# Kernel optimization log

Measured on AMD Instinct MI355X. Metric: run time of the kernel, lower is better.

## Reference

```python
import jax, jax.numpy as jnp
import numpy as np

INV_SCALE = 1.0 / (0.5 * 9)  # module's inv_scale_factor; qk is DIVIDED by this (i.e. * 4.5)


def setup_inputs() -> dict:
    key0 = jax.random.key(0)
    ks = jax.random.split(key0, 8)
    B, Sq, Sk, D, Dv = 8, 2048, 2048, 128, 256
    return {
        "query": jax.random.normal(ks[0], (B, Sq, D), dtype=jnp.float32),
        "key": jax.random.normal(ks[1], (B, Sk, D), dtype=jnp.float32),
        "value": jax.random.normal(ks[2], (B, Sk, Dv), dtype=jnp.float32),
        "mask": jax.random.normal(ks[3], (B, Sq, Sk), dtype=jnp.float32),
        # Linear weights stored torch-style as [out_features, in_features]
        "W0": jax.random.normal(ks[4], (D, D), dtype=jnp.float32) * (1.0 / np.sqrt(D)),
        "W1": jax.random.normal(ks[5], (D, D), dtype=jnp.float32) * (1.0 / np.sqrt(D)),
        "W2": jax.random.normal(ks[6], (D, Dv), dtype=jnp.float32) * (1.0 / np.sqrt(Dv)),
        "Wout": jax.random.normal(ks[7], (Dv, D), dtype=jnp.float32) * (1.0 / np.sqrt(D)),
    }


def reference(query, key, value, mask, W0, W1, W2, Wout):
    r1 = jnp.einsum("bqd,od->bqo", query, W0)          # [B,Sq,128]
    r2 = jnp.einsum("bkd,od->bko", key, W1)            # [B,Sk,128]
    r3 = jnp.einsum("bkv,ov->bko", value, W2)          # [B,Sk,128]
    qk = jnp.einsum("bqd,bkd->bqk", r1, r2)            # [B,Sq,Sk]
    scaled_qk = qk / INV_SCALE
    softmax_qk = jax.nn.softmax(scaled_qk, axis=-1)
    # dropout is identity in eval mode (deterministic reference)
    v1 = jnp.einsum("bqk,bko->bqo", softmax_qk, r3)    # [B,Sq,128]
    v2 = jnp.einsum("bqo,vo->bqv", v1, Wout)           # [B,Sq,256]
    output = v2 + jnp.einsum("bqk,bkv->bqv", mask, value)
    return output
```

## Files before the change

kernel.cpp:

```cpp
#include <hip/hip_runtime.h>
#include <cstdint>

typedef __attribute__((ext_vector_type(8))) __bf16 bf16x8;
typedef __attribute__((ext_vector_type(4))) __bf16 bf16x4;
typedef __attribute__((ext_vector_type(4))) float f32x4;

#define MFMA16(a, b, c) __builtin_amdgcn_mfma_f32_16x16x32_bf16((a), (b), (c), 0, 0, 0)
#define WAITV(N) asm volatile("s_waitcnt vmcnt(" #N ")" ::: "memory")

static constexpr int SEQ = 2048;
static constexpr int DV = 256;
static constexpr float QK_SCALE = 4.5f;

__device__ __forceinline__ bf16x4 cvt4(float4 v) {
    bf16x4 y;
    y[0] = (__bf16)v.x; y[1] = (__bf16)v.y; y[2] = (__bf16)v.z; y[3] = (__bf16)v.w;
    return y;
}

__device__ __forceinline__ void gl_lds16(const void* g, void* l) {
    __builtin_amdgcn_global_load_lds((const __attribute__((address_space(1))) uint32_t*)g,
                                     (__attribute__((address_space(3))) uint32_t*)l, 16, 0, 0);
}

template <int K, int TRANS>
__global__ __launch_bounds__(256) void k_proj(const float* __restrict__ X,
                                              const float* __restrict__ W,
                                              __bf16* __restrict__ out,
                                              float outScale) {
    __shared__ __bf16 ldsX[64][136];
    __shared__ __bf16 ldsW[128][136];

    const int t = threadIdx.x;
    const int m0 = blockIdx.x * 64;
    const int w = t >> 6, l = t & 63, lrow = l & 15, lq = l >> 4;

    f32x4 acc[8];
#pragma unroll
    for (int i = 0; i < 8; ++i) acc[i] = f32x4{0.f, 0.f, 0.f, 0.f};

#pragma unroll
    for (int kh = 0; kh < K / 128; ++kh) {
        if (kh) __syncthreads();
#pragma unroll
        for (int i = 0; i < 8; ++i) {
            int idx = t + i * 256;
            int r = idx >> 5, c4 = idx & 31;
            float4 v = *(const float4*)(X + (size_t)(m0 + r) * K + kh * 128 + c4 * 4);
            *(bf16x4*)&ldsX[r][c4 * 4] = cvt4(v);
        }
#pragma unroll
        for (int i = 0; i < 16; ++i) {
            int idx = t + i * 256;
            int r = idx >> 5, c4 = idx & 31;
            float4 v = *(const float4*)(W + (size_t)r * K + kh * 128 + c4 * 4);
            *(bf16x4*)&ldsW[r][c4 * 4] = cvt4(v);
        }
        __syncthreads();

        bf16x8 aA[4];
#pragma unroll
        for (int kc = 0; kc < 4; ++kc)
            aA[kc] = *(const bf16x8*)((const char*)&ldsX[w * 16 + lrow][0] + kc * 64 + lq * 16);
#pragma unroll
        for (int nt = 0; nt < 8; ++nt) {
#pragma unroll
            for (int kc = 0; kc < 4; ++kc) {
                bf16x8 bB = *(const bf16x8*)((const char*)&ldsW[nt * 16 + lrow][0] + kc * 64 + lq * 16);
                acc[nt] = MFMA16(aA[kc], bB, acc[nt]);
            }
        }
    }

#pragma unroll
    for (int nt = 0; nt < 8; ++nt) {
        if (TRANS) {
            int gm = m0 + w * 16 + lq * 4;
            int b = gm >> 11, s = gm & 2047;
            int col = nt * 16 + lrow;
            int kt = s >> 5, s32 = s & 31;
            int slot = (s32 >> 3) ^ ((col >> 1) & 3);
            bf16x4 y;
#pragma unroll
            for (int j = 0; j < 4; ++j) y[j] = (__bf16)(acc[nt][j] * outScale);
            *(bf16x4*)(out + (((size_t)b * 64 + kt) * 128 + col) * 32 + slot * 8 + (s32 & 7)) = y;
        } else {
#pragma unroll
            for (int j = 0; j < 4; ++j) {
                int gm = m0 + w * 16 + lq * 4 + j;
                int col = nt * 16 + lrow;
                out[(size_t)gm * 128 + col] = (__bf16)(acc[nt][j] * outScale);
            }
        }
    }
}

__global__ __launch_bounds__(256) void k_vt(const float* __restrict__ V, __bf16* __restrict__ vt) {
    __shared__ __bf16 tile[64][72];
    const int t = threadIdx.x;
    const int b = blockIdx.z, s0 = blockIdx.x * 64, v0 = blockIdx.y * 64;
#pragma unroll
    for (int i = 0; i < 4; ++i) {
        int idx = t + i * 256;
        int r = idx >> 4, c4 = idx & 15;
        float4 x = *(const float4*)(V + ((size_t)b * SEQ + s0 + r) * DV + v0 + c4 * 4);
        *(bf16x4*)&tile[r][c4 * 4] = cvt4(x);
    }
    __syncthreads();
#pragma unroll
    for (int i = 0; i < 4; ++i) {
        int idx = t + i * 256;
        int vv = idx >> 4, c4 = idx & 15;
        bf16x4 y;
        y[0] = tile[c4 * 4 + 0][vv]; y[1] = tile[c4 * 4 + 1][vv];
        y[2] = tile[c4 * 4 + 2][vv]; y[3] = tile[c4 * 4 + 3][vv];
        int v = v0 + vv;
        int kt = (s0 >> 5) + (c4 >> 3);
        int slot = ((c4 >> 1) & 3) ^ ((v >> 1) & 3);
        *(bf16x4*)(vt + (((size_t)b * 64 + kt) * 256 + v) * 32 + slot * 8 + (c4 & 1) * 4) = y;
    }
}

__global__ __launch_bounds__(256) void k_cvt_bf16(const float* __restrict__ src,
                                                  __bf16* __restrict__ dst, int n4) {
    int i = blockIdx.x * 256 + threadIdx.x;
    if (i < n4) {
        float4 v = *(const float4*)(src + (size_t)i * 4);
        *(bf16x4*)(dst + (size_t)i * 4) = cvt4(v);
    }
}

__global__ __launch_bounds__(256) void k_flash(const __bf16* __restrict__ r1s,
                                               const __bf16* __restrict__ r2,
                                               const __bf16* __restrict__ r3p,
                                               __bf16* __restrict__ v1) {
    __shared__ __align__(16) __bf16 r2s[4][32 * 128];
    __shared__ __align__(16) __bf16 r3s[4][128 * 32];
    __shared__ __bf16 plds[4][16][48];

    const int t = threadIdx.x;
    const int bx = (int)((blockIdx.x & 7) * 32 + (blockIdx.x >> 3));
    const int b = bx >> 5, q0 = (bx & 31) * 64;
    const int w = t >> 6, l = t & 63, lrow = l & 15, lq = l >> 4;

    const __bf16* r1b = r1s + (size_t)b * SEQ * 128;
    const __bf16* r2b = r2 + (size_t)b * SEQ * 128;
    const __bf16* r3b = r3p + (size_t)b * 64 * 128 * 32;

    bf16x8 aQ[4];
    {
        const __bf16* p = r1b + (size_t)(q0 + w * 16 + lrow) * 128 + lq * 8;
#pragma unroll
        for (int kc = 0; kc < 4; ++kc) aQ[kc] = *(const bf16x8*)(p + kc * 32);
    }

    const __bf16* p_r2[2];
    const __bf16* p_r3[2];
#pragma unroll
    for (int q1 = 0; q1 < 2; ++q1) {
        int r = 8 * w + 4 * q1 + (l >> 4);
        int c = (l & 15) ^ (r & 15);
        p_r2[q1] = r2b + (size_t)r * 128 + c * 8;
        p_r3[q1] = r3b + (size_t)(2 * w + q1) * 512 + l * 8;
    }

    auto stage = [&](int bi) {
#pragma unroll
        for (int q1 = 0; q1 < 2; ++q1) {
            gl_lds16(p_r2[q1], &r2s[bi][(2 * w + q1) * 512]);
            gl_lds16(p_r3[q1], &r3s[bi][(2 * w + q1) * 512]);
            p_r2[q1] += 32 * 128;
            p_r3[q1] += 128 * 32;
        }
    };

    f32x4 acc[8];
#pragma unroll
    for (int i = 0; i < 8; ++i) acc[i] = f32x4{0.f, 0.f, 0.f, 0.f};
    float mrow[4] = {-INFINITY, -INFINITY, -INFINITY, -INFINITY};
    float lsum[4] = {0.f, 0.f, 0.f, 0.f};

    stage(0); stage(1); stage(2);
    for (int it = 0; it < 64; ++it) {
        if (it < 62) { WAITV(8); } else if (it == 62) { WAITV(4); } else { WAITV(0); }
        __builtin_amdgcn_s_barrier();
        __builtin_amdgcn_sched_barrier(0);
        if (it + 3 < 64) stage((it + 3) & 3);
        __builtin_amdgcn_sched_barrier(0);
        const __bf16* R2 = &r2s[it & 3][0];
        const __bf16* R3 = &r3s[it & 3][0];

        f32x4 sc[2];
#pragma unroll
        for (int ct = 0; ct < 2; ++ct) {
            f32x4 s = f32x4{0.f, 0.f, 0.f, 0.f};
#pragma unroll
            for (int kc = 0; kc < 4; ++kc) {
                int p = (kc * 4 + lq) ^ lrow;
                bf16x8 bb = *(const bf16x8*)&R2[(ct * 16 + lrow) * 128 + p * 8];
                s = MFMA16(aQ[kc], bb, s);
            }
            sc[ct] = s;
        }

        float pm[4], ps[4], al[4];
#pragma unroll
        for (int j = 0; j < 4; ++j) pm[j] = fmaxf(sc[0][j], sc[1][j]);
#pragma unroll
        for (int off = 1; off <= 8; off <<= 1)
#pragma unroll
            for (int j = 0; j < 4; ++j) pm[j] = fmaxf(pm[j], __shfl_xor(pm[j], off, 64));
#pragma unroll
        for (int j = 0; j < 4; ++j) {
            float mn = fmaxf(mrow[j], pm[j]);
            al[j] = __expf(mrow[j] - mn);
            mrow[j] = mn;
            ps[j] = 0.f;
        }
        float pr[2][4];
#pragma unroll
        for (int ct = 0; ct < 2; ++ct)
#pragma unroll
            for (int j = 0; j < 4; ++j) {
                float p = __expf(sc[ct][j] - mrow[j]);
                pr[ct][j] = p;
                ps[j] += p;
            }
#pragma unroll
        for (int off = 1; off <= 8; off <<= 1)
#pragma unroll
            for (int j = 0; j < 4; ++j) ps[j] += __shfl_xor(ps[j], off, 64);
#pragma unroll
        for (int j = 0; j < 4; ++j) lsum[j] = lsum[j] * al[j] + ps[j];
#pragma unroll
        for (int ot = 0; ot < 8; ++ot)
#pragma unroll
            for (int j = 0; j < 4; ++j) acc[ot][j] *= al[j];

#pragma unroll
        for (int ct = 0; ct < 2; ++ct)
#pragma unroll
            for (int j = 0; j < 4; ++j)
                plds[w][lq * 4 + j][ct * 16 + lrow] = (__bf16)pr[ct][j];
        __builtin_amdgcn_s_waitcnt(0xc07f);
        bf16x8 pA = *(const bf16x8*)&plds[w][lrow][lq * 8];

#pragma unroll
        for (int ot = 0; ot < 8; ++ot) {
            int p = lq ^ ((lrow >> 1) & 3);
            bf16x8 bb = *(const bf16x8*)&R3[(ot * 16 + lrow) * 32 + p * 8];
            acc[ot] = MFMA16(pA, bb, acc[ot]);
        }
    }

#pragma unroll
    for (int ot = 0; ot < 8; ++ot)
#pragma unroll
        for (int j = 0; j < 4; ++j) {
            int q = q0 + w * 16 + lq * 4 + j;
            float v = acc[ot][j] / lsum[j];
            v1[((size_t)b * SEQ + q) * 128 + ot * 16 + lrow] = (__bf16)v;
        }
}

__global__ __launch_bounds__(512, 4) void k_out(const float* __restrict__ mask,
                                                const __bf16* __restrict__ vtp,
                                                const __bf16* __restrict__ v1,
                                                const __bf16* __restrict__ wob,
                                                float* __restrict__ out) {
    __shared__ __align__(16) __bf16 vbuf[3][256 * 32];
    __shared__ __align__(16) float mbuf[3][32 * 64];

    const int t = threadIdx.x;
    const int bid = (int)((blockIdx.x & 7) * 64 + (blockIdx.x >> 3));
    const int m0 = bid * 32;
    const int b = m0 >> 11, q0 = m0 & 2047;
    const int w = t >> 6, l = t & 63, lrow = l & 15, lq = l >> 4;
    const int rg = w & 1, cg = w >> 1;

    f32x4 acc[4];
#pragma unroll
    for (int i = 0; i < 4; ++i) acc[i] = f32x4{0.f, 0.f, 0.f, 0.f};

    const __bf16* vsrc[4];
    const float* msrc[2];
    if (w < 4) {
#pragma unroll
        for (int i = 0; i < 4; ++i)
            vsrc[i] = vtp + (size_t)b * 64 * 8192 + (w * 4 + i) * 512 + l * 8;
    } else {
        const int m = w - 4;
#pragma unroll
        for (int s = 0; s < 2; ++s) {
            int r = 4 * (m * 2 + s) + (l >> 4);
            int c = (l & 15) ^ (r & 7);
            msrc[s] = mask + ((size_t)(b * 2048 + q0 + r)) * 2048 + c * 4;
        }
    }

    if (w < 4) {
#pragma unroll
        for (int kt = 0; kt < 2; ++kt)
#pragma unroll
            for (int i = 0; i < 4; ++i)
                gl_lds16(vsrc[i] + (size_t)kt * 8192, &vbuf[kt][(w * 4 + i) * 512]);
    } else {
        const int m = w - 4;
#pragma unroll
        for (int s = 0; s < 2; ++s)
            gl_lds16(msrc[s], &mbuf[0][(m * 2 + s) * 256]);
    }

    for (int it = 0; it < 64; ++it) {
        if (w >= 4) {
            const int m = w - 4;
            if (it <= 61) {
                int e = (it >> 1) + 1, s = it & 1;
                gl_lds16(msrc[s] + (size_t)e * 64, &mbuf[e % 3][(m * 2 + s) * 256]);
            }
            if ((it & 1) == 0) {
                if (it <= 60) { WAITV(1); } else { WAITV(0); }
            }
        } else {
            if (it < 63) { WAITV(4); } else { WAITV(0); }
        }
        __builtin_amdgcn_s_barrier();
        __builtin_amdgcn_sched_barrier(0);
        if (w < 4 && it + 2 < 64) {
            int kt = it + 2;
#pragma unroll
            for (int i = 0; i < 4; ++i)
                gl_lds16(vsrc[i] + (size_t)kt * 8192, &vbuf[kt % 3][(w * 4 + i) * 512]);
        }
        __builtin_amdgcn_sched_barrier(0);

        const float* Mb = &mbuf[(it >> 1) % 3][0];
        const __bf16* V = &vbuf[it % 3][0];
        const int h = it & 1;
        int c0 = (h * 8 + lq * 2) ^ (lrow & 7);
        int c1 = (h * 8 + lq * 2 + 1) ^ (lrow & 7);
        float4 f0 = *(const float4*)&Mb[(rg * 16 + lrow) * 64 + c0 * 4];
        float4 f1 = *(const float4*)&Mb[(rg * 16 + lrow) * 64 + c1 * 4];
        bf16x8 aM;
        aM[0] = (__bf16)f0.x; aM[1] = (__bf16)f0.y; aM[2] = (__bf16)f0.z; aM[3] = (__bf16)f0.w;
        aM[4] = (__bf16)f1.x; aM[5] = (__bf16)f1.y; aM[6] = (__bf16)f1.z; aM[7] = (__bf16)f1.w;

        const int pv = lq ^ ((lrow >> 1) & 3);
#pragma unroll
        for (int vt8 = 0; vt8 < 4; ++vt8) {
            bf16x8 bb = *(const bf16x8*)&V[(cg * 64 + vt8 * 16 + lrow) * 32 + pv * 8];
            acc[vt8] = MFMA16(aM, bb, acc[vt8]);
        }
    }

    bf16x8 aV[4];
#pragma unroll
    for (int oc = 0; oc < 4; ++oc)
        aV[oc] = *(const bf16x8*)(v1 + (size_t)(m0 + rg * 16 + lrow) * 128 + oc * 32 + lq * 8);
#pragma unroll
    for (int vt8 = 0; vt8 < 4; ++vt8) {
#pragma unroll
        for (int oc = 0; oc < 4; ++oc) {
            bf16x8 bb = *(const bf16x8*)(wob + (size_t)(cg * 64 + vt8 * 16 + lrow) * 128 + oc * 32 + lq * 8);
            acc[vt8] = MFMA16(aV[oc], bb, acc[vt8]);
        }
    }

#pragma unroll
    for (int vt8 = 0; vt8 < 4; ++vt8)
#pragma unroll
        for (int j = 0; j < 4; ++j) {
            int gq = m0 + rg * 16 + lq * 4 + j;
            out[(size_t)gq * 256 + cg * 64 + vt8 * 16 + lrow] = acc[vt8][j];
        }
}

extern "C" void kernel_launch(void* const* d_in, const int* in_sizes, int n_in,
                              void* d_out, int out_size, void* d_ws, size_t ws_size,
                              hipStream_t stream) {
    const float* q    = (const float*)d_in[0];
    const float* k    = (const float*)d_in[1];
    const float* v    = (const float*)d_in[2];
    const float* mask = (const float*)d_in[3];
    const float* W0   = (const float*)d_in[4];
    const float* W1   = (const float*)d_in[5];
    const float* W2   = (const float*)d_in[6];
    const float* Wout = (const float*)d_in[7];
    float* out = (float*)d_out;

    char* ws = (char*)d_ws;
    __bf16* r1s = (__bf16*)(ws);
    __bf16* r2b = (__bf16*)(ws + (4ull << 20));
    __bf16* r3t = (__bf16*)(ws + (8ull << 20));
    __bf16* vtb = (__bf16*)(ws + (12ull << 20));
    __bf16* wob = (__bf16*)(ws + (20ull << 20));
    __bf16* v1b = (__bf16*)(ws + (21ull << 20));

    k_proj<128, 0><<<256, 256, 0, stream>>>(q, W0, r1s, QK_SCALE);
    k_proj<128, 0><<<256, 256, 0, stream>>>(k, W1, r2b, 1.0f);
    k_proj<256, 1><<<256, 256, 0, stream>>>(v, W2, r3t, 1.0f);
    k_vt<<<dim3(32, 4, 8), 256, 0, stream>>>(v, vtb);
    k_cvt_bf16<<<32, 256, 0, stream>>>(Wout, wob, 8192);
    k_flash<<<256, 256, 0, stream>>>(r1s, r2b, r3t, v1b);
    k_out<<<512, 512, 0, stream>>>(mask, vtb, v1b, wob, out);
}
```

Baseline: 393.0 us.

## Split flash attention over two key halves and merge partials in a combine kernel

Splits the flash-attention kernel along the key dimension into two halves, which doubles the grid from 256 to 512 blocks so more compute units have work. Each half writes a partial normalized output plus its row max and row sum, and a new combine kernel rescales and merges the two partials. The per-iteration row-sum shuffle reduction is also moved out of the loop, so it runs once at the end. This costs an extra kernel launch, extra global traffic for the partial outputs, and one more bf16 rounding step.

```diff
diff --git a/kernel.cpp b/kernel.cpp
--- a/kernel.cpp
+++ b/kernel.cpp
@@ -133,19 +133,20 @@
 __global__ __launch_bounds__(256) void k_flash(const __bf16* __restrict__ r1s,
                                                const __bf16* __restrict__ r2,
                                                const __bf16* __restrict__ r3p,
-                                               __bf16* __restrict__ v1) {
+                                               __bf16* __restrict__ v1p,
+                                               float* __restrict__ ml) {
     __shared__ __align__(16) __bf16 r2s[4][32 * 128];
     __shared__ __align__(16) __bf16 r3s[4][128 * 32];
     __shared__ __bf16 plds[4][16][48];
 
     const int t = threadIdx.x;
-    const int bx = (int)((blockIdx.x & 7) * 32 + (blockIdx.x >> 3));
-    const int b = bx >> 5, q0 = (bx & 31) * 64;
+    const int bx = (int)((blockIdx.x & 7) * 64 + (blockIdx.x >> 3));
+    const int b = bx >> 6, rem = bx & 63, q0 = (rem >> 1) * 64, kh = rem & 1;
     const int w = t >> 6, l = t & 63, lrow = l & 15, lq = l >> 4;
 
     const __bf16* r1b = r1s + (size_t)b * SEQ * 128;
-    const __bf16* r2b = r2 + (size_t)b * SEQ * 128;
-    const __bf16* r3b = r3p + (size_t)b * 64 * 128 * 32;
+    const __bf16* r2b = r2 + (size_t)b * SEQ * 128 + (size_t)kh * 1024 * 128;
+    const __bf16* r3b = r3p + (size_t)b * 64 * 128 * 32 + (size_t)kh * 32 * 128 * 32;
 
     bf16x8 aQ[4];
     {
@@ -181,11 +182,11 @@
     float lsum[4] = {0.f, 0.f, 0.f, 0.f};
 
     stage(0); stage(1); stage(2);
-    for (int it = 0; it < 64; ++it) {
-        if (it < 62) { WAITV(8); } else if (it == 62) { WAITV(4); } else { WAITV(0); }
+    for (int it = 0; it < 32; ++it) {
+        if (it < 30) { WAITV(8); } else if (it == 30) { WAITV(4); } else { WAITV(0); }
         __builtin_amdgcn_s_barrier();
         __builtin_amdgcn_sched_barrier(0);
-        if (it + 3 < 64) stage((it + 3) & 3);
+        if (it + 3 < 32) stage((it + 3) & 3);
         __builtin_amdgcn_sched_barrier(0);
         const __bf16* R2 = &r2s[it & 3][0];
         const __bf16* R3 = &r3s[it & 3][0];
@@ -203,7 +204,7 @@
             sc[ct] = s;
         }
 
-        float pm[4], ps[4], al[4];
+        float pm[4], al[4];
 #pragma unroll
         for (int j = 0; j < 4; ++j) pm[j] = fmaxf(sc[0][j], sc[1][j]);
 #pragma unroll
@@ -215,23 +216,16 @@
             float mn = fmaxf(mrow[j], pm[j]);
             al[j] = __expf(mrow[j] - mn);
             mrow[j] = mn;
-            ps[j] = 0.f;
         }
         float pr[2][4];
 #pragma unroll
         for (int ct = 0; ct < 2; ++ct)
 #pragma unroll
-            for (int j = 0; j < 4; ++j) {
-                float p = __expf(sc[ct][j] - mrow[j]);
-                pr[ct][j] = p;
-                ps[j] += p;
-            }
-#pragma unroll
-        for (int off = 1; off <= 8; off <<= 1)
-#pragma unroll
-            for (int j = 0; j < 4; ++j) ps[j] += __shfl_xor(ps[j], off, 64);
-#pragma unroll
-        for (int j = 0; j < 4; ++j) lsum[j] = lsum[j] * al[j] + ps[j];
+            for (int j = 0; j < 4; ++j)
+                pr[ct][j] = __expf(sc[ct][j] - mrow[j]);
+#pragma unroll
+        for (int j = 0; j < 4; ++j)
+            lsum[j] = lsum[j] * al[j] + pr[0][j] + pr[1][j];
 #pragma unroll
         for (int ot = 0; ot < 8; ++ot)
 #pragma unroll
@@ -254,13 +248,47 @@
     }
 
 #pragma unroll
+    for (int off = 1; off <= 8; off <<= 1)
+#pragma unroll
+        for (int j = 0; j < 4; ++j) lsum[j] += __shfl_xor(lsum[j], off, 64);
+
+    __bf16* vp = v1p + (size_t)kh * 8 * SEQ * 128;
+#pragma unroll
     for (int ot = 0; ot < 8; ++ot)
 #pragma unroll
         for (int j = 0; j < 4; ++j) {
             int q = q0 + w * 16 + lq * 4 + j;
             float v = acc[ot][j] / lsum[j];
-            v1[((size_t)b * SEQ + q) * 128 + ot * 16 + lrow] = (__bf16)v;
-        }
+            vp[((size_t)b * SEQ + q) * 128 + ot * 16 + lrow] = (__bf16)v;
+        }
+    if (lrow == 0) {
+#pragma unroll
+        for (int j = 0; j < 4; ++j) {
+            size_t row = (size_t)b * SEQ + q0 + w * 16 + lq * 4 + j;
+            ml[((size_t)kh * 8 * SEQ + row) * 2 + 0] = mrow[j];
+            ml[((size_t)kh * 8 * SEQ + row) * 2 + 1] = lsum[j];
+        }
+    }
+}
+
+__global__ __launch_bounds__(256) void k_comb(const __bf16* __restrict__ v1p,
+                                              const float* __restrict__ ml,
+                                              __bf16* __restrict__ v1) {
+    const int NROW = 8 * SEQ;
+    int idx = blockIdx.x * 256 + threadIdx.x;
+    int row = idx >> 4, c8 = (idx & 15) * 8;
+    float m0 = ml[(size_t)row * 2 + 0], l0 = ml[(size_t)row * 2 + 1];
+    float m1 = ml[((size_t)NROW + row) * 2 + 0], l1 = ml[((size_t)NROW + row) * 2 + 1];
+    float M = fmaxf(m0, m1);
+    float w0 = l0 * __expf(m0 - M), w1 = l1 * __expf(m1 - M);
+    float inv = 1.f / (w0 + w1);
+    w0 *= inv; w1 *= inv;
+    bf16x8 a = *(const bf16x8*)(v1p + (size_t)row * 128 + c8);
+    bf16x8 bb = *(const bf16x8*)(v1p + ((size_t)NROW + row) * 128 + c8);
+    bf16x8 o;
+#pragma unroll
+    for (int j = 0; j < 8; ++j) o[j] = (__bf16)((float)a[j] * w0 + (float)bb[j] * w1);
+    *(bf16x8*)(v1 + (size_t)row * 128 + c8) = o;
 }
 
 __global__ __launch_bounds__(512, 4) void k_out(const float* __restrict__ mask,
@@ -395,12 +423,15 @@
     __bf16* vtb = (__bf16*)(ws + (12ull << 20));
     __bf16* wob = (__bf16*)(ws + (20ull << 20));
     __bf16* v1b = (__bf16*)(ws + (21ull << 20));
+    __bf16* v1p = (__bf16*)(ws + (25ull << 20));
+    float*  mlb = (float*)(ws + (33ull << 20));
 
     k_proj<128, 0><<<256, 256, 0, stream>>>(q, W0, r1s, QK_SCALE);
     k_proj<128, 0><<<256, 256, 0, stream>>>(k, W1, r2b, 1.0f);
     k_proj<256, 1><<<256, 256, 0, stream>>>(v, W2, r3t, 1.0f);
     k_vt<<<dim3(32, 4, 8), 256, 0, stream>>>(v, vtb);
     k_cvt_bf16<<<32, 256, 0, stream>>>(Wout, wob, 8192);
-    k_flash<<<256, 256, 0, stream>>>(r1s, r2b, r3t, v1b);
+    k_flash<<<512, 256, 0, stream>>>(r1s, r2b, r3t, v1p, mlb);
+    k_comb<<<1024, 256, 0, stream>>>(v1p, mlb, v1b);
     k_out<<<512, 512, 0, stream>>>(mask, vtb, v1b, wob, out);
 }
```

Result: faster. 349.1 us (-11.2%).
